# Kernel tuning notes

Measured on AMD Instinct MI355X. Metric: run time of the kernel, lower is better.

Reference implementation:

```python
import jax, jax.numpy as jnp
import numpy as np

N_NODES = 50000
N_EDGES = 800000
IN_FEAT = 128
HIDDEN = 128
NUM_CLASS = 40


def setup_inputs() -> dict:
    key = jax.random.key(0)
    ks = jax.random.split(key, 8)
    feat = jax.random.normal(ks[0], (N_NODES, IN_FEAT), dtype=jnp.float32)
    # Glorot-ish init scale for reference weights
    W1 = jax.random.normal(ks[1], (IN_FEAT, HIDDEN), dtype=jnp.float32) / np.sqrt(IN_FEAT)
    b1 = jnp.zeros((HIDDEN,), dtype=jnp.float32)
    W2 = jax.random.normal(ks[2], (HIDDEN, HIDDEN), dtype=jnp.float32) / np.sqrt(HIDDEN)
    b2 = jnp.zeros((HIDDEN,), dtype=jnp.float32)
    W3 = jax.random.normal(ks[3], (HIDDEN, NUM_CLASS), dtype=jnp.float32) / np.sqrt(HIDDEN)
    b3 = jnp.zeros((NUM_CLASS,), dtype=jnp.float32)
    src = jax.random.randint(ks[4], (N_EDGES,), 0, N_NODES, dtype=jnp.int32)
    dst = jax.random.randint(ks[5], (N_EDGES,), 0, N_NODES, dtype=jnp.int32)
    return {"feat": feat, "W1": W1, "b1": b1, "W2": W2, "b2": b2,
            "W3": W3, "b3": b3, "src": src, "dst": dst}


def reference(feat, W1, b1, W2, b2, W3, b3, src, dst):
    # symmetric 'both' normalization as in DGL GraphConv:
    # h_dst = deg_in(dst)^{-1/2} * sum_{e:(s->d)} deg_out(s)^{-1/2} * (x_s W) + b
    ones = jnp.ones((src.shape[0],), dtype=feat.dtype)
    out_deg = jax.ops.segment_sum(ones, src, num_segments=N_NODES)
    in_deg = jax.ops.segment_sum(ones, dst, num_segments=N_NODES)
    out_norm = jax.lax.rsqrt(jnp.maximum(out_deg, 1.0))  # [N]
    in_norm = jax.lax.rsqrt(jnp.maximum(in_deg, 1.0))    # [N]

    def gconv(h, W, b):
        h = (h * out_norm[:, None]) @ W                  # [N, d_out]
        agg = jax.ops.segment_sum(h[src], dst, num_segments=N_NODES)
        return agg * in_norm[:, None] + b

    # eval mode: BatchNorm disabled (identity), dropout is a no-op
    h = jax.nn.relu(gconv(feat, W1, b1))
    h = jax.nn.relu(gconv(h, W2, b2))
    return gconv(h, W3, b3)
```

## Files before the change

### kernel.cpp

```cpp
#include <hip/hip_runtime.h>
#include <hip/hip_bf16.h>

#define N_NODES 50000
#define N_EDGES 800000
#define FEAT    128
#define HID     128
#define NCLS    40
#define XPAD    50048

#define RANGE   12500
#define NRANGE  4
#define NS      16
#define SLICE   (N_EDGES / NS)
#define NBLK    49

static constexpr size_t ALIGNB = 256;
static constexpr size_t aln(size_t x){ return (x + ALIGNB - 1) & ~(ALIGNB - 1); }
static constexpr size_t OFF_ONORM   = 0;
static constexpr size_t OFF_INORM   = OFF_ONORM + aln((size_t)N_NODES * 4);
static constexpr size_t OFF_ROWPTR  = OFF_INORM + aln((size_t)N_NODES * 4);
static constexpr size_t OFF_DIN     = OFF_ROWPTR + aln((size_t)(N_NODES + 1) * 4);
static constexpr size_t OFF_BSUM    = OFF_DIN + aln((size_t)N_NODES * 4);
static constexpr size_t OFF_BOFF    = OFF_BSUM + aln(64 * 4);
static constexpr size_t OFF_WT1     = OFF_BOFF + aln(64 * 4);
static constexpr size_t OFF_WT2     = OFF_WT1 + aln((size_t)128 * 128 * 2);
static constexpr size_t OFF_WT3     = OFF_WT2 + aln((size_t)128 * 128 * 2);
static constexpr size_t OFF_ESRC    = OFF_WT3 + aln((size_t)64 * 128 * 2);
static constexpr size_t OFF_FEATB   = OFF_ESRC + aln((size_t)N_EDGES * 4);
static constexpr size_t OFF_HTMP    = OFF_FEATB + aln((size_t)XPAD * 128 * 2);
static constexpr size_t OFF_XBUF    = OFF_HTMP + aln((size_t)XPAD * 128 * 2);
static constexpr size_t OFF_PART    = OFF_HTMP;

__device__ __forceinline__ float bflo(unsigned u){
  union { unsigned i; float f; } c; c.i = u << 16; return c.f;
}
__device__ __forceinline__ float bfhi(unsigned u){
  union { unsigned i; float f; } c; c.i = u & 0xffff0000u; return c.f;
}
__device__ __forceinline__ unsigned pkbf(float a, float b){
  union { __hip_bfloat16 h; unsigned short u; } ca, cb;
  ca.h = __float2bfloat16(a); cb.h = __float2bfloat16(b);
  return ((unsigned)cb.u << 16) | (unsigned)ca.u;
}
__device__ __forceinline__ unsigned short bf1(float a){
  union { __hip_bfloat16 h; unsigned short u; } c;
  c.h = __float2bfloat16(a); return c.u;
}

typedef __attribute__((ext_vector_type(8))) short bf16x8;
typedef __attribute__((ext_vector_type(4))) float f32x4;

__global__ void k_cvt(const float* __restrict__ x, unsigned* __restrict__ o){
  int i = blockIdx.x * 256 + threadIdx.x;
  float4 v = ((const float4*)x)[i];
  uint2 r; r.x = pkbf(v.x, v.y); r.y = pkbf(v.z, v.w);
  ((uint2*)o)[i] = r;
}

template<int WC, int CTC>
__global__ void k_prep_w(const float* __restrict__ W, unsigned* __restrict__ Wt){
  int idx = blockIdx.x * 256 + threadIdx.x;
  if (idx >= CTC * 16 * 64) return;
  int c = idx >> 6, kp = idx & 63;
  float v0 = (c < WC) ? W[(size_t)(2 * kp)     * WC + c] : 0.f;
  float v1 = (c < WC) ? W[(size_t)(2 * kp + 1) * WC + c] : 0.f;
  Wt[idx] = pkbf(v0, v1);
}

__global__ __launch_bounds__(1024) void k_hist_lds(const int* __restrict__ src,
                                                   const int* __restrict__ dst,
                                                   unsigned* __restrict__ part){
  __shared__ unsigned h[RANGE];
  const int s = blockIdx.x, r = blockIdx.y, z = blockIdx.z;
  const int* __restrict__ idx = z ? src : dst;
  const int lo = r * RANGE;
  for (int i = threadIdx.x; i < RANGE; i += 1024) h[i] = 0;
  __syncthreads();
  const int e0 = s * SLICE;
  for (int e = e0 + threadIdx.x; e < e0 + SLICE; e += 1024){
    int v = idx[e] - lo;
    if ((unsigned)v < RANGE) atomicAdd(&h[v], 1u);
  }
  __syncthreads();
  unsigned* p = part + (((size_t)z * NRANGE + r) * NS + s) * RANGE;
  for (int i = threadIdx.x; i < RANGE; i += 1024) p[i] = h[i];
}

__global__ void k_reduce_norms(const unsigned* __restrict__ part,
                               unsigned* __restrict__ din,
                               float* __restrict__ inorm,
                               float* __restrict__ onorm){
  int i = blockIdx.x * 256 + threadIdx.x;
  if (i >= N_NODES) return;
  int r = i / RANGE, off = i % RANGE;
  const unsigned* pi = part + ((size_t)r * NS) * RANGE + off;
  const unsigned* po = part + (((size_t)NRANGE + r) * NS) * RANGE + off;
  unsigned si = 0, so = 0;
  #pragma unroll
  for (int s = 0; s < NS; ++s){
    si += pi[(size_t)s * RANGE];
    so += po[(size_t)s * RANGE];
  }
  din[i] = si;
  inorm[i] = rsqrtf(fmaxf((float)si, 1.0f));
  onorm[i] = rsqrtf(fmaxf((float)so, 1.0f));
}

__global__ __launch_bounds__(1024) void k_scan1(const unsigned* __restrict__ din,
                                                int* __restrict__ rowptr,
                                                unsigned* __restrict__ bsum){
  __shared__ int wsum[16];
  const int t = threadIdx.x, lane = t & 63, w = t >> 6;
  const int i = blockIdx.x * 1024 + t;
  int v = (i < N_NODES) ? (int)din[i] : 0;
  int x = v;
  #pragma unroll
  for (int off = 1; off < 64; off <<= 1){
    int y = __shfl_up(x, off, 64);
    if (lane >= off) x += y;
  }
  if (lane == 63) wsum[w] = x;
  __syncthreads();
  if (w == 0 && lane < 16){
    int s = wsum[lane];
    #pragma unroll
    for (int off = 1; off < 16; off <<= 1){
      int y = __shfl_up(s, off, 64);
      if (lane >= off) s += y;
    }
    wsum[lane] = s;
  }
  __syncthreads();
  int woff = (w > 0) ? wsum[w - 1] : 0;
  if (i < N_NODES) rowptr[i] = woff + x - v;
  if (t == 0) bsum[blockIdx.x] = (unsigned)wsum[15];
}

__global__ void k_scan2(const unsigned* __restrict__ bsum, unsigned* __restrict__ boff){
  const int t = threadIdx.x;
  int v = (t < NBLK) ? (int)bsum[t] : 0;
  int x = v;
  #pragma unroll
  for (int off = 1; off < 64; off <<= 1){
    int y = __shfl_up(x, off, 64);
    if (t >= off) x += y;
  }
  if (t < NBLK) boff[t] = (unsigned)(x - v);
  if (t == NBLK - 1) boff[NBLK] = (unsigned)x;
}

__global__ __launch_bounds__(1024) void k_scan3(int* __restrict__ rowptr,
                                                const unsigned* __restrict__ boff){
  const int i = blockIdx.x * 1024 + threadIdx.x;
  if (i < N_NODES) rowptr[i] += (int)boff[blockIdx.x];
  else if (i == N_NODES) rowptr[i] = (int)boff[NBLK];
}

__global__ void k_base(unsigned* __restrict__ part, const int* __restrict__ rowptr){
  int i = blockIdx.x * 256 + threadIdx.x;
  if (i >= N_NODES) return;
  int r = i / RANGE, off = i % RANGE;
  unsigned* p = part + ((size_t)r * NS) * RANGE + off;
  unsigned run = (unsigned)rowptr[i];
  #pragma unroll
  for (int s = 0; s < NS; ++s){
    unsigned c = p[(size_t)s * RANGE];
    p[(size_t)s * RANGE] = run;
    run += c;
  }
}

__global__ __launch_bounds__(1024) void k_scatter_lds(const int* __restrict__ src,
                                                      const int* __restrict__ dst,
                                                      const unsigned* __restrict__ part,
                                                      int* __restrict__ esrc){
  __shared__ unsigned cur[RANGE];
  const int s = blockIdx.x, r = blockIdx.y;
  const int lo = r * RANGE;
  const unsigned* p = part + ((size_t)r * NS + s) * RANGE;
  for (int i = threadIdx.x; i < RANGE; i += 1024) cur[i] = p[i];
  __syncthreads();
  const int e0 = s * SLICE;
  for (int e = e0 + threadIdx.x; e < e0 + SLICE; e += 1024){
    int v = dst[e] - lo;
    if ((unsigned)v < RANGE){
      unsigned pos = atomicAdd(&cur[v], 1u);
      esrc[pos] = src[e];
    }
  }
}

template<int CT, int WCOUT, int OUTC>
__global__ __launch_bounds__(256) void k_gemm_mfma(const unsigned short* __restrict__ xb,
                                                   const unsigned short* __restrict__ wt,
                                                   const float* __restrict__ onorm,
                                                   unsigned short* __restrict__ outb){
  __shared__ unsigned short Wl[CT * 16][136];
  const int t = threadIdx.x;
  const int lane = t & 63;
  const int w = t >> 6;
  const int ln15 = lane & 15;
  const int quad = lane >> 4;

  {
    const uint4* w4 = (const uint4*)wt;
    #pragma unroll
    for (int i = 0; i < CT; ++i){
      int idx = t + i * 256;
      int row = idx >> 4, q = idx & 15;
      *(uint4*)&Wl[row][q * 8] = w4[idx];
    }
  }
  __syncthreads();

  f32x4 acc[CT];
  #pragma unroll
  for (int ct = 0; ct < CT; ++ct) acc[ct] = (f32x4){0.f, 0.f, 0.f, 0.f};

  const unsigned short* xrow = xb + (size_t)(blockIdx.x * 64 + w * 16 + ln15) * 128;
  #pragma unroll
  for (int kp = 0; kp < 4; ++kp){
    bf16x8 a = *(const bf16x8*)(xrow + kp * 32 + quad * 8);
    #pragma unroll
    for (int ct = 0; ct < CT; ++ct){
      bf16x8 b = *(const bf16x8*)&Wl[ct * 16 + ln15][kp * 32 + quad * 8];
      acc[ct] = __builtin_amdgcn_mfma_f32_16x16x32_bf16(a, b, acc[ct], 0, 0, 0);
    }
  }

  const int rowbase = blockIdx.x * 64 + w * 16 + quad * 4;
  float o[4];
  #pragma unroll
  for (int j = 0; j < 4; ++j){
    int r = rowbase + j;
    o[j] = (r < N_NODES) ? onorm[r] : 0.f;
  }
  #pragma unroll
  for (int ct = 0; ct < CT; ++ct){
    int col = ct * 16 + ln15;
    if (WCOUT < CT * 16 && col >= WCOUT) continue;
    #pragma unroll
    for (int j = 0; j < 4; ++j){
      int r = rowbase + j;
      if (r < N_NODES)
        outb[(size_t)r * OUTC + col] = bf1(acc[ct][j] * o[j]);
    }
  }
}

template<int CW, bool RELU, bool OUTBF>
__global__ __launch_bounds__(256) void k_agg(const unsigned* __restrict__ htmp,
                                             const int* __restrict__ rowptr,
                                             const int* __restrict__ esrc,
                                             const float* __restrict__ inorm,
                                             const float* __restrict__ bias,
                                             void* __restrict__ outv){
  constexpr int CU = CW / 2;
  const int wave = threadIdx.x >> 6;
  const int lane = threadIdx.x & 63;
  const int node = blockIdx.x * 4 + wave;
  if (node >= N_NODES) return;
  const int start = rowptr[node], end = rowptr[node + 1];
  float a0 = 0.f, a1 = 0.f, b0 = 0.f, b1 = 0.f,
        c0 = 0.f, c1 = 0.f, d0 = 0.f, d1 = 0.f;
  for (int e0 = start; e0 < end; e0 += 64){
    const int n = min(64, end - e0);
    int el = (lane < n) ? esrc[e0 + lane] : 0;
    int j = 0;
    for (; j + 4 <= n; j += 4){
      int s0 = __shfl(el, j);
      int s1 = __shfl(el, j + 1);
      int s2 = __shfl(el, j + 2);
      int s3 = __shfl(el, j + 3);
      if (lane < CU){
        unsigned u0 = htmp[(size_t)s0 * CU + lane];
        unsigned u1 = htmp[(size_t)s1 * CU + lane];
        unsigned u2 = htmp[(size_t)s2 * CU + lane];
        unsigned u3 = htmp[(size_t)s3 * CU + lane];
        a0 += bflo(u0); a1 += bfhi(u0);
        b0 += bflo(u1); b1 += bfhi(u1);
        c0 += bflo(u2); c1 += bfhi(u2);
        d0 += bflo(u3); d1 += bfhi(u3);
      }
    }
    for (; j < n; ++j){
      int s0 = __shfl(el, j);
      if (lane < CU){
        unsigned u0 = htmp[(size_t)s0 * CU + lane];
        a0 += bflo(u0); a1 += bfhi(u0);
      }
    }
  }
  if (lane < CU){
    float sc = inorm[node];
    float y0 = ((a0 + b0) + (c0 + d0)) * sc + bias[2 * lane];
    float y1 = ((a1 + b1) + (c1 + d1)) * sc + bias[2 * lane + 1];
    if (RELU){ y0 = fmaxf(y0, 0.f); y1 = fmaxf(y1, 0.f); }
    if (OUTBF){
      ((unsigned*)outv)[(size_t)node * CU + lane] = pkbf(y0, y1);
    } else {
      float2 v; v.x = y0; v.y = y1;
      *(float2*)&((float*)outv)[(size_t)node * CW + 2 * lane] = v;
    }
  }
}

extern "C" void kernel_launch(void* const* d_in, const int* in_sizes, int n_in,
                              void* d_out, int out_size, void* d_ws, size_t ws_size,
                              hipStream_t stream){
  const float* feat = (const float*)d_in[0];
  const float* W1   = (const float*)d_in[1];
  const float* b1   = (const float*)d_in[2];
  const float* W2   = (const float*)d_in[3];
  const float* b2   = (const float*)d_in[4];
  const float* W3   = (const float*)d_in[5];
  const float* b3   = (const float*)d_in[6];
  const int* src = (const int*)d_in[7];
  const int* dst = (const int*)d_in[8];
  float* out = (float*)d_out;

  char* ws = (char*)d_ws;
  float*    onorm   = (float*)   (ws + OFF_ONORM);
  float*    inorm   = (float*)   (ws + OFF_INORM);
  int*      rowptr  = (int*)     (ws + OFF_ROWPTR);
  unsigned* din     = (unsigned*)(ws + OFF_DIN);
  unsigned* bsum    = (unsigned*)(ws + OFF_BSUM);
  unsigned* boff    = (unsigned*)(ws + OFF_BOFF);
  unsigned* wt1     = (unsigned*)(ws + OFF_WT1);
  unsigned* wt2     = (unsigned*)(ws + OFF_WT2);
  unsigned* wt3     = (unsigned*)(ws + OFF_WT3);
  int*      esrc    = (int*)     (ws + OFF_ESRC);
  unsigned short* featb = (unsigned short*)(ws + OFF_FEATB);
  unsigned short* htmp  = (unsigned short*)(ws + OFF_HTMP);
  unsigned short* xbuf  = (unsigned short*)(ws + OFF_XBUF);
  unsigned* part    = (unsigned*)(ws + OFF_PART);

  const int NB = (N_NODES + 255) / 256;

  k_cvt<<<6250, 256, 0, stream>>>(feat, (unsigned*)featb);
  k_prep_w<128, 8><<<32, 256, 0, stream>>>(W1, wt1);
  k_prep_w<128, 8><<<32, 256, 0, stream>>>(W2, wt2);
  k_prep_w< 40, 4><<<16, 256, 0, stream>>>(W3, wt3);

  k_hist_lds    <<<dim3(NS, NRANGE, 2), 1024, 0, stream>>>(src, dst, part);
  k_reduce_norms<<<NB, 256, 0, stream>>>(part, din, inorm, onorm);
  k_scan1       <<<NBLK, 1024, 0, stream>>>(din, rowptr, bsum);
  k_scan2       <<<1, 64, 0, stream>>>(bsum, boff);
  k_scan3       <<<NBLK, 1024, 0, stream>>>(rowptr, boff);
  k_base        <<<NB, 256, 0, stream>>>(part, rowptr);
  k_scatter_lds <<<dim3(NS, NRANGE), 1024, 0, stream>>>(src, dst, part, esrc);

  const int GB = XPAD / 64;
  const int AB = (N_NODES + 3) / 4;
  k_gemm_mfma<8, 128, 128><<<GB, 256, 0, stream>>>(featb, (unsigned short*)wt1, onorm, htmp);
  k_agg<128, true, true ><<<AB, 256, 0, stream>>>((unsigned*)htmp, rowptr, esrc, inorm, b1, xbuf);
  k_gemm_mfma<8, 128, 128><<<GB, 256, 0, stream>>>(xbuf, (unsigned short*)wt2, onorm, htmp);
  k_agg<128, true, true ><<<AB, 256, 0, stream>>>((unsigned*)htmp, rowptr, esrc, inorm, b2, xbuf);
  k_gemm_mfma<4, 40, 40><<<GB, 256, 0, stream>>>(xbuf, (unsigned short*)wt3, onorm, htmp);
  k_agg<40, false, false><<<AB, 256, 0, stream>>>((unsigned*)htmp, rowptr, esrc, inorm, b3, out);
}
```

Before: 279.4 us.

## Fuse preprocessing kernels, convert features inside GEMM, widen slices and aggregation unroll

Several changes at once. The weight-prep kernels become one launch, and the separate fp32-to-bf16 feature conversion is folded into the first GEMM, which now reads fp32 directly. Degree reduction is merged into the first scan and the base-offset pass into the third scan, cutting the launch count. The histogram slice count doubles to 32 for more parallelism, and the aggregation loop issues 8 gathers per step for more memory-level parallelism. Merging the reductions into the scans makes them read twice as many partial counters per node, and the GEMM now clamps padding rows instead of relying on a padded buffer.

```diff
diff --git a/kernel.cpp b/kernel.cpp
--- a/kernel.cpp
+++ b/kernel.cpp
@@ -10,7 +10,7 @@
 
 #define RANGE   12500
 #define NRANGE  4
-#define NS      16
+#define NS      32
 #define SLICE   (N_EDGES / NS)
 #define NBLK    49
 
@@ -19,15 +19,13 @@
 static constexpr size_t OFF_ONORM   = 0;
 static constexpr size_t OFF_INORM   = OFF_ONORM + aln((size_t)N_NODES * 4);
 static constexpr size_t OFF_ROWPTR  = OFF_INORM + aln((size_t)N_NODES * 4);
-static constexpr size_t OFF_DIN     = OFF_ROWPTR + aln((size_t)(N_NODES + 1) * 4);
-static constexpr size_t OFF_BSUM    = OFF_DIN + aln((size_t)N_NODES * 4);
+static constexpr size_t OFF_BSUM    = OFF_ROWPTR + aln((size_t)(N_NODES + 1) * 4);
 static constexpr size_t OFF_BOFF    = OFF_BSUM + aln(64 * 4);
 static constexpr size_t OFF_WT1     = OFF_BOFF + aln(64 * 4);
 static constexpr size_t OFF_WT2     = OFF_WT1 + aln((size_t)128 * 128 * 2);
 static constexpr size_t OFF_WT3     = OFF_WT2 + aln((size_t)128 * 128 * 2);
 static constexpr size_t OFF_ESRC    = OFF_WT3 + aln((size_t)64 * 128 * 2);
-static constexpr size_t OFF_FEATB   = OFF_ESRC + aln((size_t)N_EDGES * 4);
-static constexpr size_t OFF_HTMP    = OFF_FEATB + aln((size_t)XPAD * 128 * 2);
+static constexpr size_t OFF_HTMP    = OFF_ESRC + aln((size_t)N_EDGES * 4);
 static constexpr size_t OFF_XBUF    = OFF_HTMP + aln((size_t)XPAD * 128 * 2);
 static constexpr size_t OFF_PART    = OFF_HTMP;
 
@@ -50,17 +48,15 @@
 typedef __attribute__((ext_vector_type(8))) short bf16x8;
 typedef __attribute__((ext_vector_type(4))) float f32x4;
 
-__global__ void k_cvt(const float* __restrict__ x, unsigned* __restrict__ o){
-  int i = blockIdx.x * 256 + threadIdx.x;
-  float4 v = ((const float4*)x)[i];
-  uint2 r; r.x = pkbf(v.x, v.y); r.y = pkbf(v.z, v.w);
-  ((uint2*)o)[i] = r;
-}
-
-template<int WC, int CTC>
-__global__ void k_prep_w(const float* __restrict__ W, unsigned* __restrict__ Wt){
-  int idx = blockIdx.x * 256 + threadIdx.x;
-  if (idx >= CTC * 16 * 64) return;
+__global__ void k_prep_all(const float* __restrict__ W1, const float* __restrict__ W2,
+                           const float* __restrict__ W3,
+                           unsigned* __restrict__ wt1, unsigned* __restrict__ wt2,
+                           unsigned* __restrict__ wt3){
+  int b = blockIdx.x, t = threadIdx.x;
+  const float* W; unsigned* Wt; int WC; int idx;
+  if (b < 32)      { W = W1; Wt = wt1; WC = 128; idx = b * 256 + t; }
+  else if (b < 64) { W = W2; Wt = wt2; WC = 128; idx = (b - 32) * 256 + t; }
+  else             { W = W3; Wt = wt3; WC = 40;  idx = (b - 64) * 256 + t; }
   int c = idx >> 6, kp = idx & 63;
   float v0 = (c < WC) ? W[(size_t)(2 * kp)     * WC + c] : 0.f;
   float v1 = (c < WC) ? W[(size_t)(2 * kp + 1) * WC + c] : 0.f;
@@ -86,33 +82,29 @@
   for (int i = threadIdx.x; i < RANGE; i += 1024) p[i] = h[i];
 }
 
-__global__ void k_reduce_norms(const unsigned* __restrict__ part,
-                               unsigned* __restrict__ din,
-                               float* __restrict__ inorm,
-                               float* __restrict__ onorm){
-  int i = blockIdx.x * 256 + threadIdx.x;
-  if (i >= N_NODES) return;
-  int r = i / RANGE, off = i % RANGE;
-  const unsigned* pi = part + ((size_t)r * NS) * RANGE + off;
-  const unsigned* po = part + (((size_t)NRANGE + r) * NS) * RANGE + off;
-  unsigned si = 0, so = 0;
-  #pragma unroll
-  for (int s = 0; s < NS; ++s){
-    si += pi[(size_t)s * RANGE];
-    so += po[(size_t)s * RANGE];
-  }
-  din[i] = si;
-  inorm[i] = rsqrtf(fmaxf((float)si, 1.0f));
-  onorm[i] = rsqrtf(fmaxf((float)so, 1.0f));
-}
-
-__global__ __launch_bounds__(1024) void k_scan1(const unsigned* __restrict__ din,
+__global__ __launch_bounds__(1024) void k_scan1(const unsigned* __restrict__ part,
                                                 int* __restrict__ rowptr,
-                                                unsigned* __restrict__ bsum){
+                                                unsigned* __restrict__ bsum,
+                                                float* __restrict__ inorm,
+                                                float* __restrict__ onorm){
   __shared__ int wsum[16];
   const int t = threadIdx.x, lane = t & 63, w = t >> 6;
   const int i = blockIdx.x * 1024 + t;
-  int v = (i < N_NODES) ? (int)din[i] : 0;
+  int v = 0;
+  if (i < N_NODES){
+    int r = i / RANGE, off = i % RANGE;
+    const unsigned* pi = part + ((size_t)r * NS) * RANGE + off;
+    const unsigned* po = part + (((size_t)NRANGE + r) * NS) * RANGE + off;
+    unsigned si = 0, so = 0;
+    #pragma unroll 8
+    for (int s = 0; s < NS; ++s){
+      si += pi[(size_t)s * RANGE];
+      so += po[(size_t)s * RANGE];
+    }
+    inorm[i] = rsqrtf(fmaxf((float)si, 1.0f));
+    onorm[i] = rsqrtf(fmaxf((float)so, 1.0f));
+    v = (int)si;
+  }
   int x = v;
   #pragma unroll
   for (int off = 1; off < 64; off <<= 1){
@@ -150,24 +142,22 @@
 }
 
 __global__ __launch_bounds__(1024) void k_scan3(int* __restrict__ rowptr,
-                                                const unsigned* __restrict__ boff){
+                                                const unsigned* __restrict__ boff,
+                                                unsigned* __restrict__ part){
   const int i = blockIdx.x * 1024 + threadIdx.x;
-  if (i < N_NODES) rowptr[i] += (int)boff[blockIdx.x];
-  else if (i == N_NODES) rowptr[i] = (int)boff[NBLK];
-}
-
-__global__ void k_base(unsigned* __restrict__ part, const int* __restrict__ rowptr){
-  int i = blockIdx.x * 256 + threadIdx.x;
-  if (i >= N_NODES) return;
-  int r = i / RANGE, off = i % RANGE;
-  unsigned* p = part + ((size_t)r * NS) * RANGE + off;
-  unsigned run = (unsigned)rowptr[i];
-  #pragma unroll
-  for (int s = 0; s < NS; ++s){
-    unsigned c = p[(size_t)s * RANGE];
-    p[(size_t)s * RANGE] = run;
-    run += c;
-  }
+  if (i < N_NODES){
+    int rp = rowptr[i] + (int)boff[blockIdx.x];
+    rowptr[i] = rp;
+    int r = i / RANGE, off = i % RANGE;
+    unsigned* p = part + ((size_t)r * NS) * RANGE + off;
+    unsigned run = (unsigned)rp;
+    #pragma unroll 8
+    for (int s = 0; s < NS; ++s){
+      unsigned c = p[(size_t)s * RANGE];
+      p[(size_t)s * RANGE] = run;
+      run += c;
+    }
+  } else if (i == N_NODES) rowptr[i] = (int)boff[NBLK];
 }
 
 __global__ __launch_bounds__(1024) void k_scatter_lds(const int* __restrict__ src,
@@ -190,8 +180,8 @@
   }
 }
 
-template<int CT, int WCOUT, int OUTC>
-__global__ __launch_bounds__(256) void k_gemm_mfma(const unsigned short* __restrict__ xb,
+template<int CT, int WCOUT, int OUTC, bool IN_F32>
+__global__ __launch_bounds__(256) void k_gemm_mfma(const void* __restrict__ xin,
                                                    const unsigned short* __restrict__ wt,
                                                    const float* __restrict__ onorm,
                                                    unsigned short* __restrict__ outb){
@@ -217,10 +207,22 @@
   #pragma unroll
   for (int ct = 0; ct < CT; ++ct) acc[ct] = (f32x4){0.f, 0.f, 0.f, 0.f};
 
-  const unsigned short* xrow = xb + (size_t)(blockIdx.x * 64 + w * 16 + ln15) * 128;
+  const int xr = min(blockIdx.x * 64 + w * 16 + ln15, N_NODES - 1);
   #pragma unroll
   for (int kp = 0; kp < 4; ++kp){
-    bf16x8 a = *(const bf16x8*)(xrow + kp * 32 + quad * 8);
+    bf16x8 a;
+    if (IN_F32){
+      const float4* x4 = (const float4*)xin + (size_t)xr * 32;
+      float4 p0 = x4[kp * 8 + quad * 2];
+      float4 p1 = x4[kp * 8 + quad * 2 + 1];
+      union { bf16x8 v; unsigned u[4]; } ua;
+      ua.u[0] = pkbf(p0.x, p0.y); ua.u[1] = pkbf(p0.z, p0.w);
+      ua.u[2] = pkbf(p1.x, p1.y); ua.u[3] = pkbf(p1.z, p1.w);
+      a = ua.v;
+    } else {
+      const unsigned short* xrow = (const unsigned short*)xin + (size_t)xr * 128;
+      a = *(const bf16x8*)(xrow + kp * 32 + quad * 8);
+    }
     #pragma unroll
     for (int ct = 0; ct < CT; ++ct){
       bf16x8 b = *(const bf16x8*)&Wl[ct * 16 + ln15][kp * 32 + quad * 8];
@@ -261,40 +263,48 @@
   const int node = blockIdx.x * 4 + wave;
   if (node >= N_NODES) return;
   const int start = rowptr[node], end = rowptr[node + 1];
-  float a0 = 0.f, a1 = 0.f, b0 = 0.f, b1 = 0.f,
-        c0 = 0.f, c1 = 0.f, d0 = 0.f, d1 = 0.f;
+  float aL[4] = {0.f, 0.f, 0.f, 0.f};
+  float aH[4] = {0.f, 0.f, 0.f, 0.f};
   for (int e0 = start; e0 < end; e0 += 64){
     const int n = min(64, end - e0);
     int el = (lane < n) ? esrc[e0 + lane] : 0;
     int j = 0;
+    for (; j + 8 <= n; j += 8){
+      int ss[8];
+      #pragma unroll
+      for (int q = 0; q < 8; ++q) ss[q] = __shfl(el, j + q);
+      if (lane < CU){
+        unsigned uu[8];
+        #pragma unroll
+        for (int q = 0; q < 8; ++q) uu[q] = htmp[(size_t)ss[q] * CU + lane];
+        #pragma unroll
+        for (int q = 0; q < 8; ++q){ aL[q & 3] += bflo(uu[q]); aH[q & 3] += bfhi(uu[q]); }
+      }
+    }
     for (; j + 4 <= n; j += 4){
-      int s0 = __shfl(el, j);
-      int s1 = __shfl(el, j + 1);
-      int s2 = __shfl(el, j + 2);
-      int s3 = __shfl(el, j + 3);
+      int ss[4];
+      #pragma unroll
+      for (int q = 0; q < 4; ++q) ss[q] = __shfl(el, j + q);
       if (lane < CU){
-        unsigned u0 = htmp[(size_t)s0 * CU + lane];
-        unsigned u1 = htmp[(size_t)s1 * CU + lane];
-        unsigned u2 = htmp[(size_t)s2 * CU + lane];
-        unsigned u3 = htmp[(size_t)s3 * CU + lane];
-        a0 += bflo(u0); a1 += bfhi(u0);
-        b0 += bflo(u1); b1 += bfhi(u1);
-        c0 += bflo(u2); c1 += bfhi(u2);
-        d0 += bflo(u3); d1 += bfhi(u3);
+        unsigned uu[4];
+        #pragma unroll
+        for (int q = 0; q < 4; ++q) uu[q] = htmp[(size_t)ss[q] * CU + lane];
+        #pragma unroll
+        for (int q = 0; q < 4; ++q){ aL[q] += bflo(uu[q]); aH[q] += bfhi(uu[q]); }
       }
     }
     for (; j < n; ++j){
       int s0 = __shfl(el, j);
       if (lane < CU){
         unsigned u0 = htmp[(size_t)s0 * CU + lane];
-        a0 += bflo(u0); a1 += bfhi(u0);
+        aL[0] += bflo(u0); aH[0] += bfhi(u0);
       }
     }
   }
   if (lane < CU){
     float sc = inorm[node];
-    float y0 = ((a0 + b0) + (c0 + d0)) * sc + bias[2 * lane];
-    float y1 = ((a1 + b1) + (c1 + d1)) * sc + bias[2 * lane + 1];
+    float y0 = ((aL[0] + aL[1]) + (aL[2] + aL[3])) * sc + bias[2 * lane];
+    float y1 = ((aH[0] + aH[1]) + (aH[2] + aH[3])) * sc + bias[2 * lane + 1];
     if (RELU){ y0 = fmaxf(y0, 0.f); y1 = fmaxf(y1, 0.f); }
     if (OUTBF){
       ((unsigned*)outv)[(size_t)node * CU + lane] = pkbf(y0, y1);
@@ -323,39 +333,29 @@
   float*    onorm   = (float*)   (ws + OFF_ONORM);
   float*    inorm   = (float*)   (ws + OFF_INORM);
   int*      rowptr  = (int*)     (ws + OFF_ROWPTR);
-  unsigned* din     = (unsigned*)(ws + OFF_DIN);
   unsigned* bsum    = (unsigned*)(ws + OFF_BSUM);
   unsigned* boff    = (unsigned*)(ws + OFF_BOFF);
   unsigned* wt1     = (unsigned*)(ws + OFF_WT1);
   unsigned* wt2     = (unsigned*)(ws + OFF_WT2);
   unsigned* wt3     = (unsigned*)(ws + OFF_WT3);
   int*      esrc    = (int*)     (ws + OFF_ESRC);
-  unsigned short* featb = (unsigned short*)(ws + OFF_FEATB);
-  unsigned short* htmp  = (unsigned short*)(ws + OFF_HTMP);
-  unsigned short* xbuf  = (unsigned short*)(ws + OFF_XBUF);
+  unsigned short* htmp = (unsigned short*)(ws + OFF_HTMP);
+  unsigned short* xbuf = (unsigned short*)(ws + OFF_XBUF);
   unsigned* part    = (unsigned*)(ws + OFF_PART);
 
-  const int NB = (N_NODES + 255) / 256;
-
-  k_cvt<<<6250, 256, 0, stream>>>(feat, (unsigned*)featb);
-  k_prep_w<128, 8><<<32, 256, 0, stream>>>(W1, wt1);
-  k_prep_w<128, 8><<<32, 256, 0, stream>>>(W2, wt2);
-  k_prep_w< 40, 4><<<16, 256, 0, stream>>>(W3, wt3);
-
+  k_prep_all    <<<80, 256, 0, stream>>>(W1, W2, W3, wt1, wt2, wt3);
   k_hist_lds    <<<dim3(NS, NRANGE, 2), 1024, 0, stream>>>(src, dst, part);
-  k_reduce_norms<<<NB, 256, 0, stream>>>(part, din, inorm, onorm);
-  k_scan1       <<<NBLK, 1024, 0, stream>>>(din, rowptr, bsum);
+  k_scan1       <<<NBLK, 1024, 0, stream>>>(part, rowptr, bsum, inorm, onorm);
   k_scan2       <<<1, 64, 0, stream>>>(bsum, boff);
-  k_scan3       <<<NBLK, 1024, 0, stream>>>(rowptr, boff);
-  k_base        <<<NB, 256, 0, stream>>>(part, rowptr);
+  k_scan3       <<<NBLK, 1024, 0, stream>>>(rowptr, boff, part);
   k_scatter_lds <<<dim3(NS, NRANGE), 1024, 0, stream>>>(src, dst, part, esrc);
 
   const int GB = XPAD / 64;
   const int AB = (N_NODES + 3) / 4;
-  k_gemm_mfma<8, 128, 128><<<GB, 256, 0, stream>>>(featb, (unsigned short*)wt1, onorm, htmp);
+  k_gemm_mfma<8, 128, 128, true ><<<GB, 256, 0, stream>>>(feat, (unsigned short*)wt1, onorm, htmp);
   k_agg<128, true, true ><<<AB, 256, 0, stream>>>((unsigned*)htmp, rowptr, esrc, inorm, b1, xbuf);
-  k_gemm_mfma<8, 128, 128><<<GB, 256, 0, stream>>>(xbuf, (unsigned short*)wt2, onorm, htmp);
+  k_gemm_mfma<8, 128, 128, false><<<GB, 256, 0, stream>>>(xbuf, (unsigned short*)wt2, onorm, htmp);
   k_agg<128, true, true ><<<AB, 256, 0, stream>>>((unsigned*)htmp, rowptr, esrc, inorm, b2, xbuf);
-  k_gemm_mfma<4, 40, 40><<<GB, 256, 0, stream>>>(xbuf, (unsigned short*)wt3, onorm, htmp);
+  k_gemm_mfma<4, 40, 40, false><<<GB, 256, 0, stream>>>(xbuf, (unsigned short*)wt3, onorm, htmp);
   k_agg<40, false, false><<<AB, 256, 0, stream>>>((unsigned*)htmp, rowptr, esrc, inorm, b3, out);
 }
```

Result: faster. 248.7 us (-11.0%).
